# Kernel tuning notes

Measured on AMD Instinct MI355X. Metric: run time of the kernel, lower is better.

Reference implementation:

```python
import jax, jax.numpy as jnp
import numpy as np

B, N, K, G = 8, 2048, 20, 8
EPS = 1e-5

def lrelu(v):
    return jnp.where(v >= 0, v, 0.2 * v)

def group_norm(x, gamma, beta):
    # x: (B, C, ...); normalize over channel groups and spatial dims
    b, c = x.shape[0], x.shape[1]
    xg = x.reshape(b, G, c // G, -1)
    mu = xg.mean(axis=(2, 3), keepdims=True)
    var = xg.var(axis=(2, 3), keepdims=True)
    xn = ((xg - mu) * jax.lax.rsqrt(var + EPS)).reshape(x.shape)
    sh = (1, c) + (1,) * (x.ndim - 2)
    return xn * gamma.reshape(sh) + beta.reshape(sh)

def graph_feature(x, k):
    # x: (B, C, N) -> edge features (B, 2C, N, k)
    inner = 2.0 * jnp.einsum('bcn,bcm->bnm', x, x)
    xx = jnp.sum(x * x, axis=1)                     # (B, N)
    pd = -(xx[:, :, None] - inner + xx[:, None, :]) # negative squared dist
    idx = jax.lax.top_k(pd, k)[1]                   # (B, N, k) nearest
    xt = jnp.swapaxes(x, 1, 2)                      # (B, N, C)
    nbr = jax.vmap(lambda f, i: f[i])(xt, idx)      # (B, N, k, C) gather
    ctr = jnp.broadcast_to(xt[:, :, None, :], nbr.shape)
    feat = jnp.concatenate([nbr - ctr, ctr], axis=-1)  # (B, N, k, 2C)
    return jnp.transpose(feat, (0, 3, 1, 2))

def edge_block(x, w, b, g, h):
    f = graph_feature(x, K)
    y = jnp.einsum('oc,bcnk->bonk', w, f) + b[None, :, None, None]
    return lrelu(group_norm(y, g, h)).max(axis=-1)   # (B, out, N)

def _forward(x, w0, b0, g0, h0, w1, b1, g1, h1, w2, b2, g2, h2,
             w3, b3, g3, h3, fw0, fb0, fw1, fb1, fw2, fb2):
    cur = jnp.swapaxes(x, 1, 2)                      # (B, 3, N)
    res = []
    for (w, b, g, h) in ((w0, b0, g0, h0), (w1, b1, g1, h1), (w2, b2, g2, h2)):
        cur = edge_block(cur, w, b, g, h)
        res.append(cur)
    xc = jnp.concatenate(res, axis=1)                # (B, 256, N)
    pf = jnp.einsum('oc,bcn->bon', w3, xc) + b3[None, :, None]
    pf = lrelu(group_norm(pf, g3, h3))               # (B, 256, N)
    v = jnp.concatenate([pf.max(axis=-1), pf.mean(axis=-1)], axis=1)  # (B, 512)
    v = lrelu(v @ fw0.T + fb0)
    v = lrelu(v @ fw1.T + fb1)
    return v @ fw2.T + fb2                           # (B, 256)

def setup_inputs():
    key = jax.random.key(0)
    ks = jax.random.split(key, 16)
    def rn(k, shape, s=0.05):
        return jax.random.normal(k, shape, jnp.float32) * s
    inp = {'x': jax.random.normal(ks[0], (B, N, 3), jnp.float32)}
    inp.update(w0=rn(ks[1], (64, 6)), b0=rn(ks[2], (64,)), g0=jnp.ones((64,)), h0=jnp.zeros((64,)))
    inp.update(w1=rn(ks[3], (64, 128)), b1=rn(ks[4], (64,)), g1=jnp.ones((64,)), h1=jnp.zeros((64,)))
    inp.update(w2=rn(ks[5], (128, 128)), b2=rn(ks[6], (128,)), g2=jnp.ones((128,)), h2=jnp.zeros((128,)))
    inp.update(w3=rn(ks[7], (256, 256)), b3=rn(ks[8], (256,)), g3=jnp.ones((256,)), h3=jnp.zeros((256,)))
    inp.update(fw0=rn(ks[9], (512, 512)), fb0=rn(ks[10], (512,)))
    inp.update(fw1=rn(ks[11], (512, 512)), fb1=rn(ks[12], (512,)))
    inp.update(fw2=rn(ks[13], (256, 512)), fb2=rn(ks[14], (256,)))
    return inp

def reference(x, w0, b0, g0, h0, w1, b1, g1, h1, w2, b2, g2, h2,
              w3, b3, g3, h3, fw0, fb0, fw1, fb1, fw2, fb2):
    return _forward(x, w0, b0, g0, h0, w1, b1, g1, h1, w2, b2, g2, h2,
                    w3, b3, g3, h3, fw0, fb0, fw1, fb1, fw2, fb2)
```

## Files before the change

### kernel.cpp

```cpp
#include <hip/hip_runtime.h>
#include <hip/hip_bf16.h>
#include <cstdint>


constexpr int B = 8, N = 2048, KNN = 20, G = 8;
constexpr int BN = B * N;
constexpr float EPS = 1e-5f;

using bf16 = __hip_bfloat16;
using u64 = unsigned long long;

__device__ __forceinline__ float lrelu(float v){ return v >= 0.f ? v : 0.2f * v; }
__device__ __forceinline__ unsigned fenc(float f){ unsigned u = __float_as_uint(f); return (u & 0x80000000u) ? ~u : (u | 0x80000000u); }
__device__ __forceinline__ float fdec(unsigned u){ return (u & 0x80000000u) ? __uint_as_float(u & 0x7FFFFFFFu) : __uint_as_float(~u); }

template<int NB>
__device__ __forceinline__ void batcher_sort(unsigned* s){
  #pragma unroll
  for (int p = 1; p < NB; p <<= 1){
    #pragma unroll
    for (int k = p; k >= 1; k >>= 1){
      #pragma unroll
      for (int j = k % p; j <= NB-1-k; j += 2*k){
        #pragma unroll
        for (int i = 0; i <= ((k-1 < NB-1-j-k) ? k-1 : NB-1-j-k); ++i){
          if ((i + j) / (2*p) == (i + j + k) / (2*p)){
            const unsigned lo = min(s[i+j], s[i+j+k]);
            const unsigned hi = max(s[i+j], s[i+j+k]);
            s[i+j] = lo; s[i+j+k] = hi;
          }
        }
      }
    }
  }
}

template<int NB>
__device__ __forceinline__ void topk_update(unsigned* L, const unsigned* s){
  #pragma unroll
  for (int i = 0; i < NB; ++i) L[i] = min(L[i], s[i]);
  #pragma unroll
  for (int gap = 16; gap >= 1; gap >>= 1){
    #pragma unroll
    for (int i = 0; i < 32; ++i){
      if ((i & ((gap<<1)-1)) < gap){
        const unsigned hi = max(L[i], L[i+gap]);
        const unsigned lo = min(L[i], L[i+gap]);
        L[i] = hi; L[i+gap] = lo;
      }
    }
  }
}

__device__ __forceinline__ u64 knn_dec8(unsigned kk, int q, int half){
  const unsigned ord = kk & 255u;
  const unsigned gidx = (unsigned)(half*8 + (ord >> 4))*128u + (unsigned)q + 8u*(ord & 15u);
  return ((u64)(kk & 0xFFFFFF00u) << 24) | gidx;
}

__device__ __forceinline__ void knn_merge_out(unsigned char* ovl, const unsigned* L,
    u64* __restrict__ kn2, size_t bp, int r0, int sr, int sq, int half){
  unsigned* mbuf = (unsigned*)ovl;
  #pragma unroll
  for (int k = 0; k < KNN; ++k) mbuf[(sr*8 + sq)*KNN + k] = L[31-k];
  __syncthreads();
  if (sq == 0){
    int h[8]; u64 v[8];
    #pragma unroll
    for (int q = 0; q < 8; ++q){ h[q] = 0; v[q] = knn_dec8(mbuf[(sr*8+q)*KNN], q, half); }
    u64* outp = &kn2[((bp + r0 + sr)*2 + half)*KNN];
    for (int k = 0; k < KNN; ++k){
      int best = 0; u64 bv = v[0];
      #pragma unroll
      for (int q = 1; q < 8; ++q) if (v[q] < bv){ bv = v[q]; best = q; }
      outp[k] = bv;
      #pragma unroll
      for (int q = 0; q < 8; ++q) if (q == best){
        ++h[q];
        v[q] = (h[q] < KNN) ? knn_dec8(mbuf[(sr*8+q)*KNN + h[q]], q, half) : ~0ULL;
      }
    }
  }
}

__global__ __launch_bounds__(256) void knn_fin(const u64* __restrict__ kn2, int* __restrict__ kn){
  const int p = blockIdx.x*256 + threadIdx.x;
  const u64* la = &kn2[(size_t)p*2*KNN];
  const u64* lb = la + KNN;
  int* outp = &kn[(size_t)p*KNN];
  int ia = 0, ib = 0;
  for (int k = 0; k < KNN; ++k){
    const u64 a = la[ia], c = lb[ib];
    if (a <= c){ outp[k] = (int)(unsigned)(a & 0xFFFFu); ++ia; }
    else       { outp[k] = (int)(unsigned)(c & 0xFFFFu); ++ib; }
  }
}

struct SrcPtrs { const void* p[23]; };

__global__ __launch_bounds__(256) void convert_kernel(SrcPtrs sp, float* __restrict__ dst,
                                                      float* gstat, unsigned* vmax, float* vmean){
  if (blockIdx.y == 23){
    int t = blockIdx.x * 256 + threadIdx.x;
    if (t < 512) gstat[t] = 0.f;
    if (t < B*256){ vmax[t] = 0x007FFFFFu; vmean[t] = 0.f; }
    return;
  }
  constexpr int CNT[23] = {49152,384,64,64,64,8192,64,64,64,16384,128,128,128,
                           65536,256,256,256,262144,512,262144,512,131072,256};
  constexpr int OFF[23] = {0,49152,49536,49600,49664,49728,57920,57984,58048,58112,
                           74496,74624,74752,74880,140416,140672,140928,141184,
                           403328,403840,665984,666496,797568};
  const int ti = blockIdx.y;
  const int cnt = CNT[ti], off = OFF[ti];
  const unsigned g0w = *(const unsigned*)sp.p[3];
  const bool isbf = (g0w & 0xFFFFu) == 0x3F80u;
  const float* fs = (const float*)sp.p[ti];
  const unsigned short* bs = (const unsigned short*)sp.p[ti];
  for (int j = blockIdx.x*256 + threadIdx.x; j < cnt; j += gridDim.x*256){
    dst[off + j] = isbf ? __uint_as_float((unsigned)bs[j] << 16) : fs[j];
  }
}

template<int C>
__global__ __launch_bounds__(256) void sqnorm_cm(const float* __restrict__ f, float* __restrict__ cn){
  const int p = blockIdx.x*256 + threadIdx.x;
  float s = 0.f;
  #pragma unroll 8
  for (int c = 0; c < C; ++c){ const float v = f[(size_t)c*BN + p]; s += v*v; }
  cn[p] = s;
}

template<int C>
__global__ __launch_bounds__(256) void knn_kernel(const float* __restrict__ feat, const float* __restrict__ cnG,
                                                  u64* __restrict__ kn2){
  constexpr int ROWS = 32, CT = 128, DTP = 133;
  constexpr int COLF_BYTES = C*CT*4;
  __shared__ __align__(16) unsigned char ovl[COLF_BYTES];
  __shared__ __align__(16) float rowfT[C][ROWS];
  float* colfT = (float*)ovl;
  float* dbuf  = (float*)ovl;

  const int t = threadIdx.x;
  const int b = blockIdx.y;
  const int half = blockIdx.z;
  const int r0 = blockIdx.x * ROWS;
  const size_t bp = (size_t)b * N;
  const int rg = (t & 7)*4;
  const int cg = (t >> 3)*4;
  const int sr = t >> 3;
  const int sq = t & 7;
  const float rn = cnG[bp + r0 + sr];

  for (int i = t; i < C*(ROWS/4); i += 256){
    const int c = i >> 3, r4 = (i & 7)*4;
    *(float4*)&rowfT[c][r4] = *(const float4*)&feat[(size_t)c*BN + bp + r0 + r4];
  }

  unsigned L[32];
  #pragma unroll
  for (int k = 0; k < 32; ++k) L[k] = 0xFFFFFFFFu;

  for (int ct = 0; ct < 8; ++ct){
    const int m0 = (half*8 + ct) * CT;
    __syncthreads();
    for (int i = t; i < C*(CT/4); i += 256){
      const int c = i >> 5, m4 = (i & 31)*4;
      *(float4*)&colfT[c*CT + m4] = *(const float4*)&feat[(size_t)c*BN + bp + m0 + m4];
    }
    const float4 cn4 = *(const float4*)&cnG[bp + m0 + cg];
    __syncthreads();

    float acc[4][4];
    #pragma unroll
    for (int i=0;i<4;i++){
      #pragma unroll
      for (int j=0;j<4;j++) acc[i][j]=0.f; }
    for (int c = 0; c < C; ++c){
      float4 ar = *(const float4*)&rowfT[c][rg];
      float4 cl = *(const float4*)&colfT[c*CT + cg];
      acc[0][0]+=ar.x*cl.x; acc[0][1]+=ar.x*cl.y; acc[0][2]+=ar.x*cl.z; acc[0][3]+=ar.x*cl.w;
      acc[1][0]+=ar.y*cl.x; acc[1][1]+=ar.y*cl.y; acc[1][2]+=ar.y*cl.z; acc[1][3]+=ar.y*cl.w;
      acc[2][0]+=ar.z*cl.x; acc[2][1]+=ar.z*cl.y; acc[2][2]+=ar.z*cl.z; acc[2][3]+=ar.z*cl.w;
      acc[3][0]+=ar.w*cl.x; acc[3][1]+=ar.w*cl.y; acc[3][2]+=ar.w*cl.z; acc[3][3]+=ar.w*cl.w;
    }
    __syncthreads();
    #pragma unroll
    for (int i=0;i<4;i++){
      float4 s;
      s.x = cn4.x - 2.f*acc[i][0]; s.y = cn4.y - 2.f*acc[i][1];
      s.z = cn4.z - 2.f*acc[i][2]; s.w = cn4.w - 2.f*acc[i][3];
      *(float4*)&dbuf[(rg+i)*DTP + cg] = s;
    }
    __syncthreads();

    const float* drow = &dbuf[sr*DTP];
    unsigned s16[16];
    #pragma unroll
    for (int j = 0; j < 16; ++j){
      const float d = fmaxf(drow[sq + 8*j] + rn, 0.f);
      s16[j] = (__float_as_uint(d) & 0xFFFFFF00u) | (unsigned)(ct*16 + j);
    }
    batcher_sort<16>(s16);
    topk_update<16>(L, s16);
  }

  __syncthreads();
  knn_merge_out(ovl, L, kn2, bp, r0, sr, sq, half);
}

__global__ __launch_bounds__(256) void knn3_kernel(const float* __restrict__ x, u64* __restrict__ kn2){
  constexpr int ROWS = 32, CT = 128;
  constexpr int MERGE_BYTES = ROWS*8*KNN*4;
  __shared__ __align__(16) unsigned char ovl[MERGE_BYTES];
  float* cx = (float*)ovl;
  float* cy = cx + CT;
  float* cz = cy + CT;

  const int t = threadIdx.x;
  const int b = blockIdx.y;
  const int half = blockIdx.z;
  const int r0 = blockIdx.x * ROWS;
  const size_t bp = (size_t)b * N;
  const int sr = t >> 3, sq = t & 7;
  const float rx = x[(bp + r0 + sr)*3 + 0];
  const float ry = x[(bp + r0 + sr)*3 + 1];
  const float rz = x[(bp + r0 + sr)*3 + 2];

  unsigned L[32];
  #pragma unroll
  for (int k = 0; k < 32; ++k) L[k] = 0xFFFFFFFFu;

  for (int ct = 0; ct < 8; ++ct){
    __syncthreads();
    if (t < CT){
      const size_t q = (bp + (half*8 + ct)*CT + t)*3;
      cx[t] = x[q]; cy[t] = x[q+1]; cz[t] = x[q+2];
    }
    __syncthreads();
    unsigned s16[16];
    #pragma unroll
    for (int j = 0; j < 16; ++j){
      const int m = sq + 8*j;
      const float dx = rx - cx[m], dy = ry - cy[m], dz = rz - cz[m];
      const float d = dx*dx + dy*dy + dz*dz;
      s16[j] = (__float_as_uint(d) & 0xFFFFFF00u) | (unsigned)(ct*16 + j);
    }
    batcher_sort<16>(s16);
    topk_update<16>(L, s16);
  }

  __syncthreads();
  knn_merge_out(ovl, L, kn2, bp, r0, sr, sq, half);
}

template<int C, int COUT, int MT, bool CM>
__global__ __launch_bounds__(256) void zu_kernel(const float* __restrict__ feat, const float* __restrict__ w,
                                                 const float* __restrict__ bias,
                                                 float* __restrict__ z, float* __restrict__ u){
  __shared__ __align__(16) float fT[C][MT+4];
  __shared__ __align__(16) float Wt[C][COUT+4];
  const int t = threadIdx.x;
  const size_t p0 = (size_t)blockIdx.x * MT;
  if constexpr (CM){
    for (int i = t; i < C*(MT/4); i += 256){
      const int c = i / (MT/4), m4 = (i % (MT/4))*4;
      float4 v = *(const float4*)&feat[(size_t)c*BN + p0 + m4];
      *(float4*)&fT[c][m4] = v;
    }
  } else {
    for (int i = t; i < MT*C; i += 256){ int m = i / C, c = i - m*C; fT[c][m] = feat[(p0+m)*C + c]; }
  }
  for (int i = t; i < COUT*C; i += 256){ int o = i / C, c = i - o*C; Wt[c][o] = w[o*(2*C) + c]; }
  __syncthreads();
  constexpr int MQ = MT/4;
  const int rq = t % MQ, oq = t / MQ;
  const int mm = rq*4, oo = oq*8;
  float acc[4][8];
  #pragma unroll
  for (int i=0;i<4;i++){
    #pragma unroll
    for (int j=0;j<8;j++) acc[i][j] = 0.f; }
  for (int c = 0; c < C; ++c){
    float fr[4], wv[8];
    { float4 v = *(const float4*)&fT[c][mm]; fr[0]=v.x; fr[1]=v.y; fr[2]=v.z; fr[3]=v.w; }
    { float4 v = *(const float4*)&Wt[c][oo];   wv[0]=v.x; wv[1]=v.y; wv[2]=v.z; wv[3]=v.w; }
    { float4 v = *(const float4*)&Wt[c][oo+4]; wv[4]=v.x; wv[5]=v.y; wv[6]=v.z; wv[7]=v.w; }
    #pragma unroll
    for (int i=0;i<4;i++){
      #pragma unroll
      for (int j=0;j<8;j++) acc[i][j] += fr[i]*wv[j];
    }
  }
  #pragma unroll
  for (int i=0;i<4;i++){
    float4 s0, s1;
    s0.x=acc[i][0]; s0.y=acc[i][1]; s0.z=acc[i][2]; s0.w=acc[i][3];
    s1.x=acc[i][4]; s1.y=acc[i][5]; s1.z=acc[i][6]; s1.w=acc[i][7];
    *(float4*)&z[(p0+mm+i)*COUT + oo]     = s0;
    *(float4*)&z[(p0+mm+i)*COUT + oo + 4] = s1;
  }
  __syncthreads();
  for (int i = t; i < COUT*C; i += 256){
    int o = i / C, c = i - o*C;
    Wt[c][o] = w[o*2*C + C + c] - w[o*2*C + c];
  }
  __syncthreads();
  #pragma unroll
  for (int i=0;i<4;i++){
    #pragma unroll
    for (int j=0;j<8;j++) acc[i][j] = 0.f; }
  for (int c = 0; c < C; ++c){
    float fr[4], wv[8];
    { float4 v = *(const float4*)&fT[c][mm]; fr[0]=v.x; fr[1]=v.y; fr[2]=v.z; fr[3]=v.w; }
    { float4 v = *(const float4*)&Wt[c][oo];   wv[0]=v.x; wv[1]=v.y; wv[2]=v.z; wv[3]=v.w; }
    { float4 v = *(const float4*)&Wt[c][oo+4]; wv[4]=v.x; wv[5]=v.y; wv[6]=v.z; wv[7]=v.w; }
    #pragma unroll
    for (int i=0;i<4;i++){
      #pragma unroll
      for (int j=0;j<8;j++) acc[i][j] += fr[i]*wv[j];
    }
  }
  float bb[8];
  #pragma unroll
  for (int j=0;j<8;j++) bb[j] = bias[oo+j];
  #pragma unroll
  for (int i=0;i<4;i++){
    float4 s0, s1;
    s0.x=acc[i][0]+bb[0]; s0.y=acc[i][1]+bb[1]; s0.z=acc[i][2]+bb[2]; s0.w=acc[i][3]+bb[3];
    s1.x=acc[i][4]+bb[4]; s1.y=acc[i][5]+bb[5]; s1.z=acc[i][6]+bb[6]; s1.w=acc[i][7]+bb[7];
    *(float4*)&u[(p0+mm+i)*COUT + oo]     = s0;
    *(float4*)&u[(p0+mm+i)*COUT + oo + 4] = s1;
  }
}

template<int COUT, bool MM>
__global__ __launch_bounds__(256) void edge_stats_kernel(const float* __restrict__ z, const float* __restrict__ u,
                                                         const int* __restrict__ knn, float* __restrict__ gstat,
                                                         float* __restrict__ emax, float* __restrict__ emin){
  constexpr int REPS = 256 / COUT;
  constexpr int PPT  = 16 / REPS;
  __shared__ float red[G*2];
  const int t = threadIdx.x;
  const int o = t % COUT, pr = t / COUT;
  const size_t base = (size_t)blockIdx.x * 16;
  const int b = (int)(base / N);
  if (t < G*2) red[t] = 0.f;
  __syncthreads();
  float s1 = 0.f, s2 = 0.f;
  for (int j = 0; j < PPT; ++j){
    const size_t p = base + pr + (size_t)j*REPS;
    const float uu = u[p*COUT + o];
    const int* kn = knn + p*KNN;
    float mx = -3.0e38f, mn = 3.0e38f;
    for (int k = 0; k < KNN; ++k){
      const int m = kn[k];
      const float y = z[((size_t)b*N + m)*COUT + o] + uu;
      s1 += y; s2 += y*y;
      mx = fmaxf(mx, y); mn = fminf(mn, y);
    }
    if constexpr (MM){
      emax[p*COUT + o] = mx;
      emin[p*COUT + o] = mn;
    }
  }
  const int g = o / (COUT/G);
  atomicAdd(&red[g*2+0], s1);
  atomicAdd(&red[g*2+1], s2);
  __syncthreads();
  if (t < G*2) atomicAdd(&gstat[b*(G*2) + t], red[t]);
}

__global__ __launch_bounds__(256) void edge_norm_t64(const float* __restrict__ emax, const float* __restrict__ emin,
    const float* __restrict__ gstat, const float* __restrict__ gamma, const float* __restrict__ beta,
    float* __restrict__ fout, float cntInv){
  __shared__ float tile[64][68];
  const int t = threadIdx.x;
  const size_t p0 = (size_t)blockIdx.x * 64;
  const int b = (int)(p0 / N);
  const int o4 = (t & 15) * 4;
  float sc[4], sh[4];
  #pragma unroll
  for (int e = 0; e < 4; ++e){
    const int o = o4 + e;
    const int g = o >> 3;
    const float s1 = gstat[b*16 + g*2+0], s2 = gstat[b*16 + g*2+1];
    const float mu = s1*cntInv, var = s2*cntInv - mu*mu;
    const float inv = rsqrtf(var + EPS);
    sc[e] = gamma[o]*inv; sh[e] = beta[o] - mu*sc[e];
  }
  #pragma unroll
  for (int j = 0; j < 4; ++j){
    const int p = (t >> 4) + 16*j;
    float4 mx = *(const float4*)&emax[(p0+p)*64 + o4];
    float4 mn = *(const float4*)&emin[(p0+p)*64 + o4];
    float4 r;
    r.x = lrelu(sc[0]*(sc[0]>=0.f?mx.x:mn.x)+sh[0]);
    r.y = lrelu(sc[1]*(sc[1]>=0.f?mx.y:mn.y)+sh[1]);
    r.z = lrelu(sc[2]*(sc[2]>=0.f?mx.z:mn.z)+sh[2]);
    r.w = lrelu(sc[3]*(sc[3]>=0.f?mx.w:mn.w)+sh[3]);
    *(float4*)&tile[p][o4] = r;
  }
  __syncthreads();
  const int o = t >> 2;
  #pragma unroll
  for (int jj = 0; jj < 4; ++jj){
    const int p = (t & 3)*4 + 16*jj;
    float4 r;
    r.x = tile[p+0][o]; r.y = tile[p+1][o]; r.z = tile[p+2][o]; r.w = tile[p+3][o];
    *(float4*)&fout[(size_t)o*BN + p0 + p] = r;
  }
}

template<int COUT>
__global__ __launch_bounds__(256) void edge_norm_rm(const float* __restrict__ emax, const float* __restrict__ emin,
    const float* __restrict__ gstat, const float* __restrict__ gamma, const float* __restrict__ beta,
    float* __restrict__ fout, float cntInv){
  const size_t base = ((size_t)blockIdx.x*256 + threadIdx.x)*4;
  const int o = (int)(base & (COUT-1));
  const int b = (int)(base / ((size_t)N*COUT));
  const int g = o / (COUT/G);
  const float s1 = gstat[b*(G*2) + g*2 + 0];
  const float s2 = gstat[b*(G*2) + g*2 + 1];
  const float mu  = s1 * cntInv;
  const float var = s2 * cntInv - mu*mu;
  const float inv = rsqrtf(var + EPS);
  float4 gm = *(const float4*)&gamma[o];
  float4 bt = *(const float4*)&beta[o];
  float4 mx = *(const float4*)&emax[base];
  float4 mn = *(const float4*)&emin[base];
  float4 r;
  { const float sc = gm.x*inv, sh = bt.x - mu*sc; r.x = lrelu(sc*(sc>=0.f?mx.x:mn.x)+sh); }
  { const float sc = gm.y*inv, sh = bt.y - mu*sc; r.y = lrelu(sc*(sc>=0.f?mx.y:mn.y)+sh); }
  { const float sc = gm.z*inv, sh = bt.z - mu*sc; r.z = lrelu(sc*(sc>=0.f?mx.z:mn.z)+sh); }
  { const float sc = gm.w*inv, sh = bt.w - mu*sc; r.w = lrelu(sc*(sc>=0.f?mx.w:mn.w)+sh); }
  *(float4*)&fout[base] = r;
}

template<int COUT>
__global__ __launch_bounds__(256) void edge_norm_kernel(const float* __restrict__ z, const float* __restrict__ u,
    const int* __restrict__ knn, const float* __restrict__ gstat,
    const float* __restrict__ gamma, const float* __restrict__ beta,
    float* __restrict__ fout, float cntInv){
  constexpr int REPS = 256 / COUT;
  constexpr int PPT  = 16 / REPS;
  const int t = threadIdx.x;
  const int o = t % COUT, pr = t / COUT;
  const size_t base = (size_t)blockIdx.x * 16;
  const int b = (int)(base / N);
  const int g = o / (COUT/G);
  const float s1 = gstat[b*(G*2) + g*2 + 0];
  const float s2 = gstat[b*(G*2) + g*2 + 1];
  const float mu  = s1 * cntInv;
  const float var = s2 * cntInv - mu*mu;
  const float inv = rsqrtf(var + EPS);
  const float sc = gamma[o] * inv;
  const float sh = beta[o] - mu * sc;
  for (int j = 0; j < PPT; ++j){
    const size_t p = base + pr + (size_t)j*REPS;
    const float uu = u[p*COUT + o];
    const int* kn = knn + p*KNN;
    float mx = -3.0e38f;
    for (int k = 0; k < KNN; ++k){
      const int m = kn[k];
      const float y = z[((size_t)b*N + m)*COUT + o] + uu;
      mx = fmaxf(mx, lrelu(sc*y + sh));
    }
    fout[p*COUT + o] = mx;
  }
}

__global__ __launch_bounds__(256) void conv3_kernel(const float* __restrict__ f1, const float* __restrict__ f2,
    const float* __restrict__ f3, const float* __restrict__ w3, const float* __restrict__ b3,
    float* __restrict__ y3, float* __restrict__ gstat){
  __shared__ __align__(16) float fT[32][64+4];
  __shared__ __align__(16) float Wt[32][256+4];
  __shared__ float red[G*2];
  const int t = threadIdx.x;
  const size_t p0 = (size_t)blockIdx.x * 64;
  const int b = (int)(p0 / N);
  const int rq = t & 15, oq = t >> 4;
  const int mm = rq*4, oo = oq*16;
  if (t < G*2) red[t] = 0.f;
  float acc[4][16];
  #pragma unroll
  for (int i=0;i<4;i++){
    #pragma unroll
    for (int j=0;j<16;j++) acc[i][j] = 0.f; }
  for (int cc = 0; cc < 8; ++cc){
    __syncthreads();
    if (cc < 4){
      const float* src = (cc < 2) ? f1 : f2;
      const int coff = (cc & 1)*32;
      for (int i = t; i < 512; i += 256){
        const int c = i >> 4, m4 = (i & 15)*4;
        float4 v = *(const float4*)&src[(size_t)(coff+c)*BN + p0 + m4];
        *(float4*)&fT[c][m4] = v;
      }
    } else {
      const int coff = (cc-4)*32;
      for (int i = t; i < 512; i += 256){
        const int m = i >> 3, cq = (i & 7)*4;
        float4 v = *(const float4*)&f3[(p0+m)*128 + coff + cq];
        fT[cq+0][m]=v.x; fT[cq+1][m]=v.y; fT[cq+2][m]=v.z; fT[cq+3][m]=v.w;
      }
    }
    for (int i = t; i < 2048; i += 256){
      int o = i >> 3, cq = (i & 7)*4;
      float4 v = *(const float4*)&w3[(size_t)o*256 + cc*32 + cq];
      Wt[cq+0][o]=v.x; Wt[cq+1][o]=v.y; Wt[cq+2][o]=v.z; Wt[cq+3][o]=v.w;
    }
    __syncthreads();
    for (int c = 0; c < 32; ++c){
      float fr[4], wv[16];
      { float4 v = *(const float4*)&fT[c][mm]; fr[0]=v.x; fr[1]=v.y; fr[2]=v.z; fr[3]=v.w; }
      { float4 v = *(const float4*)&Wt[c][oo+0];  wv[0]=v.x;  wv[1]=v.y;  wv[2]=v.z;  wv[3]=v.w;  }
      { float4 v = *(const float4*)&Wt[c][oo+4];  wv[4]=v.x;  wv[5]=v.y;  wv[6]=v.z;  wv[7]=v.w;  }
      { float4 v = *(const float4*)&Wt[c][oo+8];  wv[8]=v.x;  wv[9]=v.y;  wv[10]=v.z; wv[11]=v.w; }
      { float4 v = *(const float4*)&Wt[c][oo+12]; wv[12]=v.x; wv[13]=v.y; wv[14]=v.z; wv[15]=v.w; }
      #pragma unroll
      for (int i=0;i<4;i++){
        #pragma unroll
        for (int j=0;j<16;j++) acc[i][j] += fr[i]*wv[j];
      }
    }
  }
  float bb[16];
  #pragma unroll
  for (int j=0;j<16;j++) bb[j] = b3[oo+j];
  float s1 = 0.f, s2 = 0.f;
  #pragma unroll
  for (int i=0;i<4;i++){
    #pragma unroll
    for (int j=0;j<16;j++){
      acc[i][j] += bb[j];
      s1 += acc[i][j]; s2 += acc[i][j]*acc[i][j];
    }
  }
  #pragma unroll
  for (int i=0;i<4;i++){
    #pragma unroll
    for (int q=0;q<4;q++){
      float4 s;
      s.x=acc[i][q*4+0]; s.y=acc[i][q*4+1]; s.z=acc[i][q*4+2]; s.w=acc[i][q*4+3];
      *(float4*)&y3[(p0+mm+i)*256 + oo + q*4] = s;
    }
  }
  const int g = oo >> 5;
  atomicAdd(&red[g*2+0], s1);
  atomicAdd(&red[g*2+1], s2);
  __syncthreads();
  if (t < G*2) atomicAdd(&gstat[b*(G*2) + t], red[t]);
}

__global__ __launch_bounds__(256) void pf_kernel(const float* __restrict__ y3, const float* __restrict__ gstat,
    const float* __restrict__ g3, const float* __restrict__ h3,
    unsigned* __restrict__ vmax, float* __restrict__ vmean){
  const int o = threadIdx.x;
  const int b = blockIdx.y;
  const int n0 = blockIdx.x * 64;
  const int g = o >> 5;
  const float cntInv = 1.f/(32.f*N);
  const float s1 = gstat[b*(G*2)+g*2+0], s2 = gstat[b*(G*2)+g*2+1];
  const float mu = s1*cntInv, var = s2*cntInv - mu*mu;
  const float inv = rsqrtf(var + EPS);
  const float sc = g3[o] * inv;
  const float sh = h3[o] - mu*sc;
  float mx = -3.0e38f, sm = 0.f;
  for (int n = n0; n < n0+64; ++n){
    float v = y3[((size_t)b*N + n)*256 + o];
    v = lrelu(sc*v + sh);
    mx = fmaxf(mx, v);
    sm += v;
  }
  atomicMax(&vmax[b*256+o], fenc(mx));
  atomicAdd(&vmean[b*256+o], sm * (1.f/N));
}

__global__ __launch_bounds__(256) void fc_fused(const unsigned* __restrict__ vmax, const float* __restrict__ vmean,
    const float* __restrict__ fw0, const float* __restrict__ fb0,
    const float* __restrict__ fw1, const float* __restrict__ fb1,
    const float* __restrict__ fw2, const float* __restrict__ fb2,
    void* outp, const unsigned* __restrict__ dflag){
  __shared__ float va[512], vb[512];
  const int t = threadIdx.x, b = blockIdx.x;
  for (int c = t; c < 512; c += 256)
    va[c] = (c < 256) ? fdec(vmax[b*256 + c]) : vmean[b*256 + (c-256)];
  __syncthreads();
  {
    float a0 = fb0[t], a1 = fb0[t+256];
    const float* w0p = fw0 + (size_t)t*512;
    const float* w1p = fw0 + (size_t)(t+256)*512;
    for (int c = 0; c < 512; c += 4){
      float4 wa = *(const float4*)&w0p[c];
      float4 wb = *(const float4*)&w1p[c];
      a0 += wa.x*va[c+0] + wa.y*va[c+1] + wa.z*va[c+2] + wa.w*va[c+3];
      a1 += wb.x*va[c+0] + wb.y*va[c+1] + wb.z*va[c+2] + wb.w*va[c+3];
    }
    vb[t] = lrelu(a0); vb[t+256] = lrelu(a1);
  }
  __syncthreads();
  {
    float a0 = fb1[t], a1 = fb1[t+256];
    const float* w0p = fw1 + (size_t)t*512;
    const float* w1p = fw1 + (size_t)(t+256)*512;
    for (int c = 0; c < 512; c += 4){
      float4 wa = *(const float4*)&w0p[c];
      float4 wb = *(const float4*)&w1p[c];
      a0 += wa.x*vb[c+0] + wa.y*vb[c+1] + wa.z*vb[c+2] + wa.w*vb[c+3];
      a1 += wb.x*vb[c+0] + wb.y*vb[c+1] + wb.z*vb[c+2] + wb.w*vb[c+3];
    }
    va[t] = lrelu(a0); va[t+256] = lrelu(a1);
  }
  __syncthreads();
  {
    float a = fb2[t];
    const float* wp = fw2 + (size_t)t*512;
    for (int c = 0; c < 512; c += 4){
      float4 wv = *(const float4*)&wp[c];
      a += wv.x*va[c+0] + wv.y*va[c+1] + wv.z*va[c+2] + wv.w*va[c+3];
    }
    const bool isbf = ((*dflag) & 0xFFFFu) == 0x3F80u;
    if (isbf) ((bf16*)outp)[b*256 + t] = __float2bfloat16(a);
    else      ((float*)outp)[b*256 + t] = a;
  }
}

extern "C" void kernel_launch(void* const* d_in, const int* in_sizes, int n_in,
                              void* d_out, int out_size, void* d_ws, size_t ws_size,
                              hipStream_t stream){
  (void)in_sizes; (void)n_in; (void)out_size;

  float* ws = (float*)d_ws;
  float* f1 = ws;
  float* f2 = f1 + (size_t)64*BN;
  float* f3 = f2 + (size_t)64*BN;
  float* zb = f3 + (size_t)128*BN;
  float* ub = zb + (size_t)128*BN;
  int*   kn = (int*)(ub + (size_t)128*BN);
  float* gs = (float*)(kn + (size_t)BN*KNN);
  unsigned* vmax = (unsigned*)(gs + 512);
  float* vmean = (float*)(vmax + B*256);
  float* cnG = vmean + B*256;
  float* pc = cnG + (size_t)BN;
  float* y3 = zb;
  u64* kn2 = (u64*)ub;
  float* emax2 = pc + 797824;
  float* emin2 = emax2 + (size_t)128*BN;
  const size_t need2 = (size_t)((emin2 + (size_t)128*BN) - ws) * 4;
  const bool fused2 = (ws_size >= need2);
  float* emax01 = f3;
  float* emin01 = f3 + (size_t)64*BN;

  const float* xc  = pc + 0;
  const float* w0c = pc + 49152;  const float* b0c = pc + 49536;
  const float* g0c = pc + 49600;  const float* h0c = pc + 49664;
  const float* w1c = pc + 49728;  const float* b1c = pc + 57920;
  const float* g1c = pc + 57984;  const float* h1c = pc + 58048;
  const float* w2c = pc + 58112;  const float* b2c = pc + 74496;
  const float* g2c = pc + 74624;  const float* h2c = pc + 74752;
  const float* w3c = pc + 74880;  const float* b3c = pc + 140416;
  const float* g3c = pc + 140672; const float* h3c = pc + 140928;
  const float* fw0c= pc + 141184; const float* fb0c= pc + 403328;
  const float* fw1c= pc + 403840; const float* fb1c= pc + 665984;
  const float* fw2c= pc + 666496; const float* fb2c= pc + 797568;

  SrcPtrs sp;
  for (int i = 0; i < 23; ++i) sp.p[i] = d_in[i];
  convert_kernel<<<dim3(64, 24), 256, 0, stream>>>(sp, pc, gs, vmax, vmean);

  knn3_kernel<<<dim3(N/32, B, 2), 256, 0, stream>>>(xc, kn2);
  knn_fin<<<BN/256, 256, 0, stream>>>(kn2, kn);
  zu_kernel<3, 64, 128, false><<<BN/128, 256, 0, stream>>>(xc, w0c, b0c, zb, ub);
  edge_stats_kernel<64,true><<<BN/16, 256, 0, stream>>>(zb, ub, kn, gs + 0, emax01, emin01);
  edge_norm_t64<<<BN/64, 256, 0, stream>>>(emax01, emin01, gs + 0, g0c, h0c, f1, 1.f/327680.f);

  sqnorm_cm<64><<<BN/256, 256, 0, stream>>>(f1, cnG);
  knn_kernel<64><<<dim3(N/32, B, 2), 256, 0, stream>>>(f1, cnG, kn2);
  knn_fin<<<BN/256, 256, 0, stream>>>(kn2, kn);
  zu_kernel<64, 64, 128, true><<<BN/128, 256, 0, stream>>>(f1, w1c, b1c, zb, ub);
  edge_stats_kernel<64,true><<<BN/16, 256, 0, stream>>>(zb, ub, kn, gs + 128, emax01, emin01);
  edge_norm_t64<<<BN/64, 256, 0, stream>>>(emax01, emin01, gs + 128, g1c, h1c, f2, 1.f/327680.f);

  sqnorm_cm<64><<<BN/256, 256, 0, stream>>>(f2, cnG);
  knn_kernel<64><<<dim3(N/32, B, 2), 256, 0, stream>>>(f2, cnG, kn2);
  knn_fin<<<BN/256, 256, 0, stream>>>(kn2, kn);
  zu_kernel<64, 128, 64, true><<<BN/64, 256, 0, stream>>>(f2, w2c, b2c, zb, ub);
  if (fused2){
    edge_stats_kernel<128,true><<<BN/16, 256, 0, stream>>>(zb, ub, kn, gs + 256, emax2, emin2);
    edge_norm_rm<128><<<(BN*128)/1024, 256, 0, stream>>>(emax2, emin2, gs + 256, g2c, h2c, f3, 1.f/655360.f);
  } else {
    edge_stats_kernel<128,false><<<BN/16, 256, 0, stream>>>(zb, ub, kn, gs + 256, nullptr, nullptr);
    edge_norm_kernel<128><<<BN/16, 256, 0, stream>>>(zb, ub, kn, gs + 256, g2c, h2c, f3, 1.f/655360.f);
  }

  conv3_kernel<<<BN/64, 256, 0, stream>>>(f1, f2, f3, w3c, b3c, y3, gs + 384);
  pf_kernel<<<dim3(32, B), 256, 0, stream>>>(y3, gs + 384, g3c, h3c, vmax, vmean);

  fc_fused<<<B, 256, 0, stream>>>(vmax, vmean, fw0c, fb0c, fw1c, fb1c, fw2c, fb2c,
                                  d_out, (const unsigned*)d_in[3]);
}
```

Baseline: 686.8 us.

## Split KNN column range four ways and fold merge and sqnorm into consumers

The KNN kernels now split the candidate columns into four parts instead of two, which doubles the grid for more parallelism. The final merge of the per-part lists moves into edge_stats_kernel, loaded through shared memory, so knn_fin is no longer launched. The squared-norm pass is folded into edge_norm_t64 with a shared-memory atomic, which removes the sqnorm_cm launches. The four-way path needs extra workspace and falls back to the old two-way path when the workspace is too small, at the cost of more partial-list traffic and merge work.

```diff
diff --git a/kernel.cpp b/kernel.cpp
--- a/kernel.cpp
+++ b/kernel.cpp
@@ -52,23 +52,25 @@
   }
 }
 
-__device__ __forceinline__ u64 knn_dec8(unsigned kk, int q, int half){
+__device__ __forceinline__ u64 knn_dec8(unsigned kk, int q, int gtile0){
   const unsigned ord = kk & 255u;
-  const unsigned gidx = (unsigned)(half*8 + (ord >> 4))*128u + (unsigned)q + 8u*(ord & 15u);
+  const unsigned gidx = (unsigned)(gtile0 + (ord >> 4))*128u + (unsigned)q + 8u*(ord & 15u);
   return ((u64)(kk & 0xFFFFFF00u) << 24) | gidx;
 }
 
+template<int SPLIT>
 __device__ __forceinline__ void knn_merge_out(unsigned char* ovl, const unsigned* L,
-    u64* __restrict__ kn2, size_t bp, int r0, int sr, int sq, int half){
+    u64* __restrict__ kn2, size_t bp, int r0, int sr, int sq, int part){
   unsigned* mbuf = (unsigned*)ovl;
+  const int gtile0 = part * (16/SPLIT);
   #pragma unroll
   for (int k = 0; k < KNN; ++k) mbuf[(sr*8 + sq)*KNN + k] = L[31-k];
   __syncthreads();
   if (sq == 0){
     int h[8]; u64 v[8];
     #pragma unroll
-    for (int q = 0; q < 8; ++q){ h[q] = 0; v[q] = knn_dec8(mbuf[(sr*8+q)*KNN], q, half); }
-    u64* outp = &kn2[((bp + r0 + sr)*2 + half)*KNN];
+    for (int q = 0; q < 8; ++q){ h[q] = 0; v[q] = knn_dec8(mbuf[(sr*8+q)*KNN], q, gtile0); }
+    u64* outp = &kn2[((bp + r0 + sr)*SPLIT + part)*KNN];
     for (int k = 0; k < KNN; ++k){
       int best = 0; u64 bv = v[0];
       #pragma unroll
@@ -77,7 +79,7 @@
       #pragma unroll
       for (int q = 0; q < 8; ++q) if (q == best){
         ++h[q];
-        v[q] = (h[q] < KNN) ? knn_dec8(mbuf[(sr*8+q)*KNN + h[q]], q, half) : ~0ULL;
+        v[q] = (h[q] < KNN) ? knn_dec8(mbuf[(sr*8+q)*KNN + h[q]], q, gtile0) : ~0ULL;
       }
     }
   }
@@ -122,19 +124,10 @@
   }
 }
 
-template<int C>
-__global__ __launch_bounds__(256) void sqnorm_cm(const float* __restrict__ f, float* __restrict__ cn){
-  const int p = blockIdx.x*256 + threadIdx.x;
-  float s = 0.f;
-  #pragma unroll 8
-  for (int c = 0; c < C; ++c){ const float v = f[(size_t)c*BN + p]; s += v*v; }
-  cn[p] = s;
-}
-
-template<int C>
+template<int C, int SPLIT>
 __global__ __launch_bounds__(256) void knn_kernel(const float* __restrict__ feat, const float* __restrict__ cnG,
                                                   u64* __restrict__ kn2){
-  constexpr int ROWS = 32, CT = 128, DTP = 133;
+  constexpr int ROWS = 32, CT = 128, DTP = 133, TILES = 16/SPLIT;
   constexpr int COLF_BYTES = C*CT*4;
   __shared__ __align__(16) unsigned char ovl[COLF_BYTES];
   __shared__ __align__(16) float rowfT[C][ROWS];
@@ -143,7 +136,7 @@
 
   const int t = threadIdx.x;
   const int b = blockIdx.y;
-  const int half = blockIdx.z;
+  const int part = blockIdx.z;
   const int r0 = blockIdx.x * ROWS;
   const size_t bp = (size_t)b * N;
   const int rg = (t & 7)*4;
@@ -161,8 +154,8 @@
   #pragma unroll
   for (int k = 0; k < 32; ++k) L[k] = 0xFFFFFFFFu;
 
-  for (int ct = 0; ct < 8; ++ct){
-    const int m0 = (half*8 + ct) * CT;
+  for (int ct = 0; ct < TILES; ++ct){
+    const int m0 = (part*TILES + ct) * CT;
     __syncthreads();
     for (int i = t; i < C*(CT/4); i += 256){
       const int c = i >> 5, m4 = (i & 31)*4;
@@ -206,11 +199,12 @@
   }
 
   __syncthreads();
-  knn_merge_out(ovl, L, kn2, bp, r0, sr, sq, half);
-}
-
+  knn_merge_out<SPLIT>(ovl, L, kn2, bp, r0, sr, sq, part);
+}
+
+template<int SPLIT>
 __global__ __launch_bounds__(256) void knn3_kernel(const float* __restrict__ x, u64* __restrict__ kn2){
-  constexpr int ROWS = 32, CT = 128;
+  constexpr int ROWS = 32, CT = 128, TILES = 16/SPLIT;
   constexpr int MERGE_BYTES = ROWS*8*KNN*4;
   __shared__ __align__(16) unsigned char ovl[MERGE_BYTES];
   float* cx = (float*)ovl;
@@ -219,7 +213,7 @@
 
   const int t = threadIdx.x;
   const int b = blockIdx.y;
-  const int half = blockIdx.z;
+  const int part = blockIdx.z;
   const int r0 = blockIdx.x * ROWS;
   const size_t bp = (size_t)b * N;
   const int sr = t >> 3, sq = t & 7;
@@ -231,10 +225,10 @@
   #pragma unroll
   for (int k = 0; k < 32; ++k) L[k] = 0xFFFFFFFFu;
 
-  for (int ct = 0; ct < 8; ++ct){
+  for (int ct = 0; ct < TILES; ++ct){
     __syncthreads();
     if (t < CT){
-      const size_t q = (bp + (half*8 + ct)*CT + t)*3;
+      const size_t q = (bp + (part*TILES + ct)*CT + t)*3;
       cx[t] = x[q]; cy[t] = x[q+1]; cz[t] = x[q+2];
     }
     __syncthreads();
@@ -251,7 +245,7 @@
   }
 
   __syncthreads();
-  knn_merge_out(ovl, L, kn2, bp, r0, sr, sq, half);
+  knn_merge_out<SPLIT>(ovl, L, kn2, bp, r0, sr, sq, part);
 }
 
 template<int C, int COUT, int MT, bool CM>
@@ -334,27 +328,51 @@
   }
 }
 
-template<int COUT, bool MM>
+template<int COUT, bool MM, int NL>
 __global__ __launch_bounds__(256) void edge_stats_kernel(const float* __restrict__ z, const float* __restrict__ u,
-                                                         const int* __restrict__ knn, float* __restrict__ gstat,
+                                                         const int* __restrict__ knn, const u64* __restrict__ kn2,
+                                                         float* __restrict__ gstat,
                                                          float* __restrict__ emax, float* __restrict__ emin){
   constexpr int REPS = 256 / COUT;
   constexpr int PPT  = 16 / REPS;
   __shared__ float red[G*2];
+  __shared__ int kn_s[16][KNN];
+  __shared__ u64 kn2_s[(NL > 0 ? 16*NL*KNN : 1)];
   const int t = threadIdx.x;
   const int o = t % COUT, pr = t / COUT;
   const size_t base = (size_t)blockIdx.x * 16;
   const int b = (int)(base / N);
   if (t < G*2) red[t] = 0.f;
+  if constexpr (NL > 0){
+    for (int i = t; i < 16*NL*KNN; i += 256)
+      kn2_s[i] = kn2[base*NL*KNN + i];
+    __syncthreads();
+    if (t < 16){
+      int h[NL]; u64 v[NL];
+      #pragma unroll
+      for (int l = 0; l < NL; ++l){ h[l] = 0; v[l] = kn2_s[(t*NL + l)*KNN]; }
+      for (int k = 0; k < KNN; ++k){
+        int best = 0; u64 bv = v[0];
+        #pragma unroll
+        for (int l = 1; l < NL; ++l) if (v[l] < bv){ bv = v[l]; best = l; }
+        kn_s[t][k] = (int)(unsigned)(bv & 0xFFFFu);
+        #pragma unroll
+        for (int l = 0; l < NL; ++l) if (l == best){
+          ++h[l];
+          v[l] = (h[l] < KNN) ? kn2_s[(t*NL + l)*KNN + h[l]] : ~0ULL;
+        }
+      }
+    }
+  }
   __syncthreads();
   float s1 = 0.f, s2 = 0.f;
   for (int j = 0; j < PPT; ++j){
-    const size_t p = base + pr + (size_t)j*REPS;
+    const int pl = pr + j*REPS;
+    const size_t p = base + pl;
     const float uu = u[p*COUT + o];
-    const int* kn = knn + p*KNN;
     float mx = -3.0e38f, mn = 3.0e38f;
     for (int k = 0; k < KNN; ++k){
-      const int m = kn[k];
+      const int m = (NL > 0) ? kn_s[pl][k] : knn[p*KNN + k];
       const float y = z[((size_t)b*N + m)*COUT + o] + uu;
       s1 += y; s2 += y*y;
       mx = fmaxf(mx, y); mn = fminf(mn, y);
@@ -373,12 +391,14 @@
 
 __global__ __launch_bounds__(256) void edge_norm_t64(const float* __restrict__ emax, const float* __restrict__ emin,
     const float* __restrict__ gstat, const float* __restrict__ gamma, const float* __restrict__ beta,
-    float* __restrict__ fout, float cntInv){
+    float* __restrict__ fout, float* __restrict__ cnout, float cntInv){
   __shared__ float tile[64][68];
+  __shared__ float cn_s[64];
   const int t = threadIdx.x;
   const size_t p0 = (size_t)blockIdx.x * 64;
   const int b = (int)(p0 / N);
   const int o4 = (t & 15) * 4;
+  if (t < 64) cn_s[t] = 0.f;
   float sc[4], sh[4];
   #pragma unroll
   for (int e = 0; e < 4; ++e){
@@ -389,6 +409,7 @@
     const float inv = rsqrtf(var + EPS);
     sc[e] = gamma[o]*inv; sh[e] = beta[o] - mu*sc[e];
   }
+  __syncthreads();
   #pragma unroll
   for (int j = 0; j < 4; ++j){
     const int p = (t >> 4) + 16*j;
@@ -400,8 +421,10 @@
     r.z = lrelu(sc[2]*(sc[2]>=0.f?mx.z:mn.z)+sh[2]);
     r.w = lrelu(sc[3]*(sc[3]>=0.f?mx.w:mn.w)+sh[3]);
     *(float4*)&tile[p][o4] = r;
-  }
-  __syncthreads();
+    atomicAdd(&cn_s[p], r.x*r.x + r.y*r.y + r.z*r.z + r.w*r.w);
+  }
+  __syncthreads();
+  if (t < 64) cnout[p0 + t] = cn_s[t];
   const int o = t >> 2;
   #pragma unroll
   for (int jj = 0; jj < 4; ++jj){
@@ -644,11 +667,14 @@
   float* cnG = vmean + B*256;
   float* pc = cnG + (size_t)BN;
   float* y3 = zb;
-  u64* kn2 = (u64*)ub;
   float* emax2 = pc + 797824;
   float* emin2 = emax2 + (size_t)128*BN;
-  const size_t need2 = (size_t)((emin2 + (size_t)128*BN) - ws) * 4;
-  const bool fused2 = (ws_size >= need2);
+  u64* kn2d = (u64*)(emin2 + (size_t)128*BN);
+  const size_t need_f2 = (size_t)((float*)kn2d - ws) * 4;
+  const size_t need_rm = need_f2 + (size_t)BN*4*KNN*sizeof(u64);
+  const bool fused2 = (ws_size >= need_f2);
+  const bool roomy  = (ws_size >= need_rm);
+  u64* kn2f = (u64*)ub;
   float* emax01 = f3;
   float* emin01 = f3 + (size_t)64*BN;
 
@@ -669,29 +695,46 @@
   for (int i = 0; i < 23; ++i) sp.p[i] = d_in[i];
   convert_kernel<<<dim3(64, 24), 256, 0, stream>>>(sp, pc, gs, vmax, vmean);
 
-  knn3_kernel<<<dim3(N/32, B, 2), 256, 0, stream>>>(xc, kn2);
-  knn_fin<<<BN/256, 256, 0, stream>>>(kn2, kn);
-  zu_kernel<3, 64, 128, false><<<BN/128, 256, 0, stream>>>(xc, w0c, b0c, zb, ub);
-  edge_stats_kernel<64,true><<<BN/16, 256, 0, stream>>>(zb, ub, kn, gs + 0, emax01, emin01);
-  edge_norm_t64<<<BN/64, 256, 0, stream>>>(emax01, emin01, gs + 0, g0c, h0c, f1, 1.f/327680.f);
-
-  sqnorm_cm<64><<<BN/256, 256, 0, stream>>>(f1, cnG);
-  knn_kernel<64><<<dim3(N/32, B, 2), 256, 0, stream>>>(f1, cnG, kn2);
-  knn_fin<<<BN/256, 256, 0, stream>>>(kn2, kn);
-  zu_kernel<64, 64, 128, true><<<BN/128, 256, 0, stream>>>(f1, w1c, b1c, zb, ub);
-  edge_stats_kernel<64,true><<<BN/16, 256, 0, stream>>>(zb, ub, kn, gs + 128, emax01, emin01);
-  edge_norm_t64<<<BN/64, 256, 0, stream>>>(emax01, emin01, gs + 128, g1c, h1c, f2, 1.f/327680.f);
-
-  sqnorm_cm<64><<<BN/256, 256, 0, stream>>>(f2, cnG);
-  knn_kernel<64><<<dim3(N/32, B, 2), 256, 0, stream>>>(f2, cnG, kn2);
-  knn_fin<<<BN/256, 256, 0, stream>>>(kn2, kn);
-  zu_kernel<64, 128, 64, true><<<BN/64, 256, 0, stream>>>(f2, w2c, b2c, zb, ub);
-  if (fused2){
-    edge_stats_kernel<128,true><<<BN/16, 256, 0, stream>>>(zb, ub, kn, gs + 256, emax2, emin2);
+  if (roomy){
+    knn3_kernel<4><<<dim3(N/32, B, 4), 256, 0, stream>>>(xc, kn2d);
+    zu_kernel<3, 64, 128, false><<<BN/128, 256, 0, stream>>>(xc, w0c, b0c, zb, ub);
+    edge_stats_kernel<64,true,4><<<BN/16, 256, 0, stream>>>(zb, ub, nullptr, kn2d, gs + 0, emax01, emin01);
+  } else {
+    knn3_kernel<2><<<dim3(N/32, B, 2), 256, 0, stream>>>(xc, kn2f);
+    knn_fin<<<BN/256, 256, 0, stream>>>(kn2f, kn);
+    zu_kernel<3, 64, 128, false><<<BN/128, 256, 0, stream>>>(xc, w0c, b0c, zb, ub);
+    edge_stats_kernel<64,true,0><<<BN/16, 256, 0, stream>>>(zb, ub, kn, nullptr, gs + 0, emax01, emin01);
+  }
+  edge_norm_t64<<<BN/64, 256, 0, stream>>>(emax01, emin01, gs + 0, g0c, h0c, f1, cnG, 1.f/327680.f);
+
+  if (roomy){
+    knn_kernel<64,4><<<dim3(N/32, B, 4), 256, 0, stream>>>(f1, cnG, kn2d);
+    zu_kernel<64, 64, 128, true><<<BN/128, 256, 0, stream>>>(f1, w1c, b1c, zb, ub);
+    edge_stats_kernel<64,true,4><<<BN/16, 256, 0, stream>>>(zb, ub, nullptr, kn2d, gs + 128, emax01, emin01);
+  } else {
+    knn_kernel<64,2><<<dim3(N/32, B, 2), 256, 0, stream>>>(f1, cnG, kn2f);
+    knn_fin<<<BN/256, 256, 0, stream>>>(kn2f, kn);
+    zu_kernel<64, 64, 128, true><<<BN/128, 256, 0, stream>>>(f1, w1c, b1c, zb, ub);
+    edge_stats_kernel<64,true,0><<<BN/16, 256, 0, stream>>>(zb, ub, kn, nullptr, gs + 128, emax01, emin01);
+  }
+  edge_norm_t64<<<BN/64, 256, 0, stream>>>(emax01, emin01, gs + 128, g1c, h1c, f2, cnG, 1.f/327680.f);
+
+  if (roomy){
+    knn_kernel<64,4><<<dim3(N/32, B, 4), 256, 0, stream>>>(f2, cnG, kn2d);
+    zu_kernel<64, 128, 64, true><<<BN/64, 256, 0, stream>>>(f2, w2c, b2c, zb, ub);
+    edge_stats_kernel<128,true,4><<<BN/16, 256, 0, stream>>>(zb, ub, nullptr, kn2d, gs + 256, emax2, emin2);
     edge_norm_rm<128><<<(BN*128)/1024, 256, 0, stream>>>(emax2, emin2, gs + 256, g2c, h2c, f3, 1.f/655360.f);
   } else {
-    edge_stats_kernel<128,false><<<BN/16, 256, 0, stream>>>(zb, ub, kn, gs + 256, nullptr, nullptr);
-    edge_norm_kernel<128><<<BN/16, 256, 0, stream>>>(zb, ub, kn, gs + 256, g2c, h2c, f3, 1.f/655360.f);
+    knn_kernel<64,2><<<dim3(N/32, B, 2), 256, 0, stream>>>(f2, cnG, kn2f);
+    knn_fin<<<BN/256, 256, 0, stream>>>(kn2f, kn);
+    zu_kernel<64, 128, 64, true><<<BN/64, 256, 0, stream>>>(f2, w2c, b2c, zb, ub);
+    if (fused2){
+      edge_stats_kernel<128,true,0><<<BN/16, 256, 0, stream>>>(zb, ub, kn, nullptr, gs + 256, emax2, emin2);
+      edge_norm_rm<128><<<(BN*128)/1024, 256, 0, stream>>>(emax2, emin2, gs + 256, g2c, h2c, f3, 1.f/655360.f);
+    } else {
+      edge_stats_kernel<128,false,0><<<BN/16, 256, 0, stream>>>(zb, ub, kn, nullptr, gs + 256, nullptr, nullptr);
+      edge_norm_kernel<128><<<BN/16, 256, 0, stream>>>(zb, ub, kn, gs + 256, g2c, h2c, f3, 1.f/655360.f);
+    }
   }
 
   conv3_kernel<<<BN/64, 256, 0, stream>>>(f1, f2, f3, w3c, b3c, y3, gs + 384);
```

New measurement: 689.9 us. About the same (+0.5%).
